# Kernel optimization log

Hardware: AMD Instinct MI355X
Metric: run time of the kernel (lower is better)

## Reference

```python
import jax, jax.numpy as jnp
import numpy as np

N_QUBITS = 8
N_CYCLES = 4
N_GATES = 10
MEAS_QUBITS = (3, 7)
BATCH = 16384


def _apply_ry_batched(state, angles, w):
    # angles: [B] per-example RY angle on wire w. state: [B,2,...,2]
    half = angles * 0.5
    c = jnp.cos(half).astype(jnp.complex64)
    s = jnp.sin(half).astype(jnp.complex64)
    U = jnp.stack([jnp.stack([c, -s], -1), jnp.stack([s, c], -1)], -2)  # [B,2,2]
    st = jnp.moveaxis(state, w + 1, -1)
    st = jnp.einsum('bij,b...j->b...i', U, st)
    return jnp.moveaxis(st, -1, w + 1)


def _apply_cnot(state, c, t):
    st = jnp.moveaxis(state, (c + 1, t + 1), (-2, -1))
    st = jnp.concatenate([st[..., 0:1, :], st[..., 1:2, ::-1]], axis=-2)
    return jnp.moveaxis(st, (-2, -1), (c + 1, t + 1))


def _apply_crx(state, theta, c, t):
    # CRX: RX(theta) on target when control=1 (torchquantum convention)
    half = theta * 0.5
    co = jnp.cos(half).astype(jnp.complex64)
    si = (-1j * jnp.sin(half)).astype(jnp.complex64)
    st = jnp.moveaxis(state, (c + 1, t + 1), (-2, -1))
    s1 = st[..., 1, :]
    s1 = jnp.stack([co * s1[..., 0] + si * s1[..., 1],
                    si * s1[..., 0] + co * s1[..., 1]], -1)
    st = jnp.concatenate([st[..., 0:1, :], s1[..., None, :]], axis=-2)
    return jnp.moveaxis(st, (-2, -1), (c + 1, t + 1))


def _expval_z(probs, w):
    axes = tuple(a for a in range(1, N_QUBITS + 1) if a != w + 1)
    m = jnp.sum(probs, axis=axes)  # [B,2]
    return m[:, 0] - m[:, 1]


def _forward(x, crx_theta, w1, b1, w2, b2):
    B = x.shape[0]
    state = jnp.zeros((B, 2 ** N_QUBITS), jnp.complex64).at[:, 0].set(1.0)
    state = state.reshape((B,) + (2,) * N_QUBITS)
    # encoding ansatz: per cycle, RY(x[:,cyc,q]) on each qubit + CNOT ring
    for cyc in range(N_CYCLES):
        for q in range(N_QUBITS):
            state = _apply_ry_batched(state, x[:, cyc, q], q)
        for q in range(N_QUBITS):
            state = _apply_cnot(state, q, (q + 1) % N_QUBITS)
    # trainable CRX layer
    for i in range(N_GATES):
        state = _apply_crx(state, crx_theta[i], i % N_QUBITS, (i + 1) % N_QUBITS)
    probs = jnp.abs(state) ** 2  # real, [B,2,...,2]
    feats = jnp.stack([_expval_z(probs, q) for q in MEAS_QUBITS], -1)  # [B,2]
    h = jnp.tanh(feats @ w1.T + b1)
    return jax.nn.sigmoid(h @ w2.T + b2)  # [B,1]


def setup_inputs() -> dict:
    key = jax.random.key(0)
    ks = jax.random.split(key, 6)
    x = jax.random.normal(ks[0], (BATCH, N_CYCLES, N_QUBITS), jnp.float32)
    crx_theta = jax.random.normal(ks[1], (N_GATES,), jnp.float32) * 0.1
    w1 = jax.random.normal(ks[2], (10, 2), jnp.float32) * (1.0 / np.sqrt(2.0))
    b1 = jnp.zeros((10,), jnp.float32)
    w2 = jax.random.normal(ks[3], (1, 10), jnp.float32) * (1.0 / np.sqrt(10.0))
    b2 = jnp.zeros((1,), jnp.float32)
    return {"x": x, "crx_theta": crx_theta, "w1": w1, "b1": b1, "w2": w2, "b2": b2}


def reference(x, crx_theta, w1, b1, w2, b2):
    return _forward(x, crx_theta, w1, b1, w2, b2)
```

## Files before the change

kernel.cpp:

```cpp
#include <hip/hip_runtime.h>
#include <math.h>


typedef float f2 __attribute__((ext_vector_type(2)));

#define RLF(v, i) __int_as_float(__builtin_amdgcn_readlane(__float_as_int(v), (i)))
#define BPF(a, v) __int_as_float(__builtin_amdgcn_ds_bpermute((a), __float_as_int(v)))
#define DPPF(v, ctrl) __uint_as_float((unsigned)__builtin_amdgcn_update_dpp( \
    0, (int)__float_as_uint(v), (ctrl), 0xf, 0xf, true))

__device__ __forceinline__ f2 mk2(float a, float b) { f2 r; r.x = a; r.y = b; return r; }

#define PX1S(v)  DPPF((v), 0xB1)
#define PX2S(v)  DPPF((v), 0x4E)
#define PX4S(v)  DPPF(DPPF((v), 0x141), 0x1B)
#define PX8S(v)  DPPF((v), 0x128)

#define PX1(v)  mk2(PX1S((v).x), PX1S((v).y))
#define PX2(v)  mk2(PX2S((v).x), PX2S((v).y))
#define PX4(v)  mk2(PX4S((v).x), PX4S((v).y))
#define PX8(v)  mk2(PX8S((v).x), PX8S((v).y))
#define PX16(v) mk2(BPF(a16, (v).x), BPF(a16, (v).y))
#define PX32(v) mk2(BPF(a32, (v).x), BPF(a32, (v).y))
#define FMA2(a, b, c) __builtin_elementwise_fma((a), (b), (c))

__global__ __launch_bounds__(256, 8) void vqcnn_wave(
    const float* __restrict__ x,
    const float* __restrict__ crx_theta,
    const float* __restrict__ w1,
    const float* __restrict__ b1,
    const float* __restrict__ w2,
    const float* __restrict__ b2,
    float* __restrict__ out)
{
    const int lane = threadIdx.x & 63;
    const int bA   = blockIdx.x * 8 + (threadIdx.x >> 6) * 2;
    const int bB   = bA + 1;

    float cvA, svA, cvB, svB;
    {
        float angA = 0.0f, angB = 0.0f;
        if (lane < 32) {
            angA = x[bA * 32 + lane];
            angB = x[bB * 32 + lane];
        } else if (lane < 42) {
            angA = angB = crx_theta[lane - 32];
        }
        __sincosf(0.5f * angA, &svA, &cvA);
        __sincosf(0.5f * angB, &svB, &cvB);
    }

    const int a16 = (lane ^ 16) << 2;
    const int a32 = (lane ^ 32) << 2;
    const int g4  = (lane ^ (lane >> 1)) << 2;
    const int g4b = g4 ^ (48 << 2);
    const bool l0 = (lane & 1) != 0;

#define RL2C(i) mk2(RLF(cvA, (i)), RLF(cvB, (i)))
#define RL2S(i) mk2(RLF(svA, (i)), RLF(svB, (i)))

    f2 vv0, vv1, vv2, vv3;
    {
#define SEL0(bit, i) ((lane & (bit)) ? RL2S(i) : RL2C(i))
        f2 L = SEL0(32, 0) * SEL0(16, 1);
        L = L * SEL0(8, 2);
        L = L * SEL0(4, 3);
        L = L * SEL0(2, 4);
        L = L * SEL0(1, 5);
        const f2 c6 = RL2C(6), s6 = RL2S(6);
        const f2 c7 = RL2C(7), s7 = RL2S(7);
        const f2 Lc6 = L * c6, Ls6 = L * s6;
        vv0 = Lc6 * c7; vv1 = Lc6 * s7; vv2 = Ls6 * c7; vv3 = Ls6 * s7;
    }

#define RING() {                                                             \
    const f2 t0a = PXG(vv0), t0b = PXG(vv2);                                 \
    const f2 t1a = PXGB(vv1), t1b = PXGB(vv3);                               \
    const f2 t2a = PXG(vv3), t2b = PXG(vv1);                                 \
    const f2 t3a = PXGB(vv2), t3b = PXGB(vv0);                               \
    vv0 = l0 ? t0b : t0a;  vv1 = l0 ? t1b : t1a;                             \
    vv2 = l0 ? t2b : t2a;  vv3 = l0 ? t3b : t3a; }
#define PXG(v)  mk2(BPF(g4,  (v).x), BPF(g4,  (v).y))
#define PXGB(v) mk2(BPF(g4b, (v).x), BPF(g4b, (v).y))
    RING()

#define RY_G(ia, mask, PART) {                                               \
    const f2 c = RL2C(ia), s = RL2S(ia);                                     \
    const f2 ss = (lane & (mask)) ? s : -s;                                  \
    const f2 p0 = PART(vv0), p1 = PART(vv1);                                 \
    const f2 p2 = PART(vv2), p3 = PART(vv3);                                 \
    vv0 = FMA2(ss, p0, c * vv0); vv1 = FMA2(ss, p1, c * vv1);                \
    vv2 = FMA2(ss, p2, c * vv2); vv3 = FMA2(ss, p3, c * vv3); }

#define RY_SLOT1(ia) {                                                       \
    const f2 c = RL2C(ia), s = RL2S(ia);                                     \
    const f2 n0 = c*vv0 - s*vv2, n2 = FMA2(s, vv0, c*vv2);                   \
    const f2 n1 = c*vv1 - s*vv3, n3 = FMA2(s, vv1, c*vv3);                   \
    vv0 = n0; vv1 = n1; vv2 = n2; vv3 = n3; }

#define RY_SLOT0(ia) {                                                       \
    const f2 c = RL2C(ia), s = RL2S(ia);                                     \
    const f2 n0 = c*vv0 - s*vv1, n1 = FMA2(s, vv0, c*vv1);                   \
    const f2 n2 = c*vv2 - s*vv3, n3 = FMA2(s, vv2, c*vv3);                   \
    vv0 = n0; vv1 = n1; vv2 = n2; vv3 = n3; }

    #pragma unroll
    for (int cyc = 1; cyc < 4; ++cyc) {
        const int base = cyc * 8;
        RY_G(base + 0, 32, PX32)
        RY_G(base + 1, 16, PX16)
        RY_G(base + 2,  8, PX8)
        RY_G(base + 3,  4, PX4)
        RY_G(base + 4,  2, PX2)
        RY_G(base + 5,  1, PX1)
        RY_SLOT1(base + 6)
        RY_SLOT0(base + 7)
        RING()
    }

    f2 rr0 = vv0, rr1 = vv1, rr2 = vv2, rr3 = vv3;
    f2 ii0 = {0.f, 0.f}, ii1 = {0.f, 0.f}, ii2 = {0.f, 0.f}, ii3 = {0.f, 0.f};

#define CRX_G(gi, cmask, PART) {                                             \
    const f2 c = RL2C(32 + (gi)), s = RL2S(32 + (gi));                       \
    const bool ct = (lane & (cmask)) != 0;                                   \
    f2 pr, pi, nr, ni;                                                       \
    pr = PART(rr0); pi = PART(ii0);                                          \
    nr = FMA2(s, pi, c*rr0); ni = c*ii0 - s*pr;                              \
    rr0 = ct?nr:rr0; ii0 = ct?ni:ii0;                                        \
    pr = PART(rr1); pi = PART(ii1);                                          \
    nr = FMA2(s, pi, c*rr1); ni = c*ii1 - s*pr;                              \
    rr1 = ct?nr:rr1; ii1 = ct?ni:ii1;                                        \
    pr = PART(rr2); pi = PART(ii2);                                          \
    nr = FMA2(s, pi, c*rr2); ni = c*ii2 - s*pr;                              \
    rr2 = ct?nr:rr2; ii2 = ct?ni:ii2;                                        \
    pr = PART(rr3); pi = PART(ii3);                                          \
    nr = FMA2(s, pi, c*rr3); ni = c*ii3 - s*pr;                              \
    rr3 = ct?nr:rr3; ii3 = ct?ni:ii3; }

    CRX_G(0, 32, PX16)
    CRX_G(1, 16, PX8)
    CRX_G(2,  8, PX4)
    CRX_G(3,  4, PX2)
    CRX_G(4,  2, PX1)
    {
        const f2 c = RL2C(37), s = RL2S(37);
        const f2 nr0 = FMA2(s, ii2, c*rr0), ni0 = c*ii0 - s*rr2;
        const f2 nr2 = FMA2(s, ii0, c*rr2), ni2 = c*ii2 - s*rr0;
        const f2 nr1 = FMA2(s, ii3, c*rr1), ni1 = c*ii1 - s*rr3;
        const f2 nr3 = FMA2(s, ii1, c*rr3), ni3 = c*ii3 - s*rr1;
        rr0 = l0?nr0:rr0; ii0 = l0?ni0:ii0; rr1 = l0?nr1:rr1; ii1 = l0?ni1:ii1;
        rr2 = l0?nr2:rr2; ii2 = l0?ni2:ii2; rr3 = l0?nr3:rr3; ii3 = l0?ni3:ii3;
    }
    {
        const f2 c = RL2C(38), s = RL2S(38);
        const f2 nr2 = FMA2(s, ii3, c*rr2), ni2 = c*ii2 - s*rr3;
        const f2 nr3 = FMA2(s, ii2, c*rr3), ni3 = c*ii3 - s*rr2;
        rr2 = nr2; ii2 = ni2; rr3 = nr3; ii3 = ni3;
    }
    {
        const f2 c = RL2C(39), s = RL2S(39);
        const f2 pr1 = PX32(rr1), pi1 = PX32(ii1);
        const f2 pr3 = PX32(rr3), pi3 = PX32(ii3);
        const f2 nr1 = FMA2(s, pi1, c*rr1), ni1 = c*ii1 - s*pr1;
        const f2 nr3 = FMA2(s, pi3, c*rr3), ni3 = c*ii3 - s*pr3;
        rr1 = nr1; ii1 = ni1; rr3 = nr3; ii3 = ni3;
    }
    CRX_G(8, 32, PX16)
    CRX_G(9, 16, PX8)

    const f2 p0 = FMA2(rr0, rr0, ii0*ii0), p1 = FMA2(rr1, rr1, ii1*ii1);
    const f2 p2 = FMA2(rr2, rr2, ii2*ii2), p3 = FMA2(rr3, rr3, ii3*ii3);
    const f2 sum = (p0 + p1) + (p2 + p3);
    f2 vq7 = (p0 + p2) - (p1 + p3);
    f2 vq3 = (lane & 4) ? -sum : sum;
    vq3 = vq3 + PX1(vq3);   vq7 = vq7 + PX1(vq7);
    vq3 = vq3 + PX2(vq3);   vq7 = vq7 + PX2(vq7);
    vq3 = vq3 + PX4(vq3);   vq7 = vq7 + PX4(vq7);
    vq3 = vq3 + PX8(vq3);   vq7 = vq7 + PX8(vq7);
    vq3 = vq3 + PX16(vq3);  vq7 = vq7 + PX16(vq7);
    vq3 = vq3 + PX32(vq3);  vq7 = vq7 + PX32(vq7);

    float wa = 0.f, wb = 0.f, bb = 0.f, wc = 0.f;
    if (lane < 10) {
        wa = w1[2 * lane];
        wb = w1[2 * lane + 1];
        bb = b1[lane];
        wc = w2[lane];
    }
    const f2 z = FMA2(mk2(wa, wa), vq3, FMA2(mk2(wb, wb), vq7, mk2(bb, bb)));
    const f2 e = mk2(__expf(2.0f * z.x), __expf(2.0f * z.y));
    const f2 h = mk2(1.0f - 2.0f * __builtin_amdgcn_rcpf(e.x + 1.0f),
                     1.0f - 2.0f * __builtin_amdgcn_rcpf(e.y + 1.0f));
    f2 acc = mk2(wc, wc) * h;
    acc = acc + PX1(acc);
    acc = acc + PX2(acc);
    acc = acc + PX4(acc);
    acc = acc + PX8(acc);
    if (lane == 0) {
        const float bias = b2[0];
        out[bA] = __builtin_amdgcn_rcpf(1.0f + __expf(-(acc.x + bias)));
        out[bB] = __builtin_amdgcn_rcpf(1.0f + __expf(-(acc.y + bias)));
    }
}

extern "C" void kernel_launch(void* const* d_in, const int* in_sizes, int n_in,
                              void* d_out, int out_size, void* d_ws, size_t ws_size,
                              hipStream_t stream) {
    const float* x         = (const float*)d_in[0];
    const float* crx_theta = (const float*)d_in[1];
    const float* w1        = (const float*)d_in[2];
    const float* b1        = (const float*)d_in[3];
    const float* w2        = (const float*)d_in[4];
    const float* b2        = (const float*)d_in[5];
    float* out = (float*)d_out;

    const int B = in_sizes[0] / 32;
    vqcnn_wave<<<B / 8, 256, 0, stream>>>(x, crx_theta, w1, b1, w2, b2, out);
}
```

Before: 81.48 us.

## Process four batch examples per wavefront and cut ring permute selects

Each wavefront now simulates four examples instead of two, held as two interleaved f2 state sets. This doubles independent instruction streams for latency hiding and halves the grid size. The CNOT ring now selects sources by lane-parity before the bpermute, so each ring step issues half as many bpermutes. The cost is higher register pressure (launch bounds drop to 4 waves/EU) and fewer total wavefronts to fill the GPU.

```diff
diff --git a/kernel.cpp b/kernel.cpp
--- a/kernel.cpp
+++ b/kernel.cpp
@@ -24,7 +24,7 @@
 #define PX32(v) mk2(BPF(a32, (v).x), BPF(a32, (v).y))
 #define FMA2(a, b, c) __builtin_elementwise_fma((a), (b), (c))
 
-__global__ __launch_bounds__(256, 8) void vqcnn_wave(
+__global__ __launch_bounds__(256, 4) void vqcnn_wave(
     const float* __restrict__ x,
     const float* __restrict__ crx_theta,
     const float* __restrict__ w1,
@@ -34,152 +34,210 @@
     float* __restrict__ out)
 {
     const int lane = threadIdx.x & 63;
-    const int bA   = blockIdx.x * 8 + (threadIdx.x >> 6) * 2;
-    const int bB   = bA + 1;
-
-    float cvA, svA, cvB, svB;
-    {
-        float angA = 0.0f, angB = 0.0f;
+    const int bA   = blockIdx.x * 16 + (threadIdx.x >> 6) * 4;
+
+    float cvA, svA, cvB, svB, cvC, svC, cvD, svD;
+    {
+        float aA = 0.f, aB = 0.f, aC = 0.f, aD = 0.f;
         if (lane < 32) {
-            angA = x[bA * 32 + lane];
-            angB = x[bB * 32 + lane];
+            aA = x[(bA + 0) * 32 + lane];
+            aB = x[(bA + 1) * 32 + lane];
+            aC = x[(bA + 2) * 32 + lane];
+            aD = x[(bA + 3) * 32 + lane];
         } else if (lane < 42) {
-            angA = angB = crx_theta[lane - 32];
+            aA = aB = aC = aD = crx_theta[lane - 32];
         }
-        __sincosf(0.5f * angA, &svA, &cvA);
-        __sincosf(0.5f * angB, &svB, &cvB);
+        __sincosf(0.5f * aA, &svA, &cvA);
+        __sincosf(0.5f * aB, &svB, &cvB);
+        __sincosf(0.5f * aC, &svC, &cvC);
+        __sincosf(0.5f * aD, &svD, &cvD);
     }
 
     const int a16 = (lane ^ 16) << 2;
     const int a32 = (lane ^ 32) << 2;
     const int g4  = (lane ^ (lane >> 1)) << 2;
     const int g4b = g4 ^ (48 << 2);
-    const bool l0 = (lane & 1) != 0;
-
-#define RL2C(i) mk2(RLF(cvA, (i)), RLF(cvB, (i)))
-#define RL2S(i) mk2(RLF(svA, (i)), RLF(svB, (i)))
-
-    f2 vv0, vv1, vv2, vv3;
-    {
-#define SEL0(bit, i) ((lane & (bit)) ? RL2S(i) : RL2C(i))
-        f2 L = SEL0(32, 0) * SEL0(16, 1);
-        L = L * SEL0(8, 2);
-        L = L * SEL0(4, 3);
-        L = L * SEL0(2, 4);
-        L = L * SEL0(1, 5);
-        const f2 c6 = RL2C(6), s6 = RL2S(6);
-        const f2 c7 = RL2C(7), s7 = RL2S(7);
-        const f2 Lc6 = L * c6, Ls6 = L * s6;
-        vv0 = Lc6 * c7; vv1 = Lc6 * s7; vv2 = Ls6 * c7; vv3 = Ls6 * s7;
-    }
-
-#define RING() {                                                             \
-    const f2 t0a = PXG(vv0), t0b = PXG(vv2);                                 \
-    const f2 t1a = PXGB(vv1), t1b = PXGB(vv3);                               \
-    const f2 t2a = PXG(vv3), t2b = PXG(vv1);                                 \
-    const f2 t3a = PXGB(vv2), t3b = PXGB(vv0);                               \
-    vv0 = l0 ? t0b : t0a;  vv1 = l0 ? t1b : t1a;                             \
-    vv2 = l0 ? t2b : t2a;  vv3 = l0 ? t3b : t3a; }
-#define PXG(v)  mk2(BPF(g4,  (v).x), BPF(g4,  (v).y))
-#define PXGB(v) mk2(BPF(g4b, (v).x), BPF(g4b, (v).y))
-    RING()
-
-#define RY_G(ia, mask, PART) {                                               \
-    const f2 c = RL2C(ia), s = RL2S(ia);                                     \
-    const f2 ss = (lane & (mask)) ? s : -s;                                  \
-    const f2 p0 = PART(vv0), p1 = PART(vv1);                                 \
-    const f2 p2 = PART(vv2), p3 = PART(vv3);                                 \
-    vv0 = FMA2(ss, p0, c * vv0); vv1 = FMA2(ss, p1, c * vv1);                \
-    vv2 = FMA2(ss, p2, c * vv2); vv3 = FMA2(ss, p3, c * vv3); }
-
-#define RY_SLOT1(ia) {                                                       \
-    const f2 c = RL2C(ia), s = RL2S(ia);                                     \
-    const f2 n0 = c*vv0 - s*vv2, n2 = FMA2(s, vv0, c*vv2);                   \
-    const f2 n1 = c*vv1 - s*vv3, n3 = FMA2(s, vv1, c*vv3);                   \
-    vv0 = n0; vv1 = n1; vv2 = n2; vv3 = n3; }
-
-#define RY_SLOT0(ia) {                                                       \
-    const f2 c = RL2C(ia), s = RL2S(ia);                                     \
-    const f2 n0 = c*vv0 - s*vv1, n1 = FMA2(s, vv0, c*vv1);                   \
-    const f2 n2 = c*vv2 - s*vv3, n3 = FMA2(s, vv2, c*vv3);                   \
-    vv0 = n0; vv1 = n1; vv2 = n2; vv3 = n3; }
+    const bool psel = (__builtin_popcount(lane) & 1) != 0;
+
+#define RLCu(i) mk2(RLF(cvA, (i)), RLF(cvB, (i)))
+#define RLSu(i) mk2(RLF(svA, (i)), RLF(svB, (i)))
+#define RLCw(i) mk2(RLF(cvC, (i)), RLF(cvD, (i)))
+#define RLSw(i) mk2(RLF(svC, (i)), RLF(svD, (i)))
+
+    f2 vv0u, vv1u, vv2u, vv3u, vv0w, vv1w, vv2w, vv3w;
+    {
+#define SELu(bit, i) ((lane & (bit)) ? RLSu(i) : RLCu(i))
+#define SELw(bit, i) ((lane & (bit)) ? RLSw(i) : RLCw(i))
+        f2 Lu = SELu(32, 0) * SELu(16, 1);
+        f2 Lw = SELw(32, 0) * SELw(16, 1);
+        Lu = Lu * SELu(8, 2);   Lw = Lw * SELw(8, 2);
+        Lu = Lu * SELu(4, 3);   Lw = Lw * SELw(4, 3);
+        Lu = Lu * SELu(2, 4);   Lw = Lw * SELw(2, 4);
+        Lu = Lu * SELu(1, 5);   Lw = Lw * SELw(1, 5);
+        const f2 c6u = RLCu(6), s6u = RLSu(6), c7u = RLCu(7), s7u = RLSu(7);
+        const f2 c6w = RLCw(6), s6w = RLSw(6), c7w = RLCw(7), s7w = RLSw(7);
+        const f2 Lcu = Lu * c6u, Lsu = Lu * s6u;
+        const f2 Lcw = Lw * c6w, Lsw = Lw * s6w;
+        vv0u = Lcu * c7u; vv1u = Lcu * s7u; vv2u = Lsu * c7u; vv3u = Lsu * s7u;
+        vv0w = Lcw * c7w; vv1w = Lcw * s7w; vv2w = Lsw * c7w; vv3w = Lsw * s7w;
+    }
+
+#define RING2() {                                                            \
+    const f2 z0u = psel ? vv2u : vv0u,  z0w = psel ? vv2w : vv0w;            \
+    const f2 z1u = psel ? vv3u : vv1u,  z1w = psel ? vv3w : vv1w;            \
+    const f2 z2u = psel ? vv1u : vv3u,  z2w = psel ? vv1w : vv3w;            \
+    const f2 z3u = psel ? vv0u : vv2u,  z3w = psel ? vv0w : vv2w;            \
+    vv0u = mk2(BPF(g4,  z0u.x), BPF(g4,  z0u.y));                            \
+    vv0w = mk2(BPF(g4,  z0w.x), BPF(g4,  z0w.y));                            \
+    vv1u = mk2(BPF(g4b, z1u.x), BPF(g4b, z1u.y));                            \
+    vv1w = mk2(BPF(g4b, z1w.x), BPF(g4b, z1w.y));                            \
+    vv2u = mk2(BPF(g4,  z2u.x), BPF(g4,  z2u.y));                            \
+    vv2w = mk2(BPF(g4,  z2w.x), BPF(g4,  z2w.y));                            \
+    vv3u = mk2(BPF(g4b, z3u.x), BPF(g4b, z3u.y));                            \
+    vv3w = mk2(BPF(g4b, z3w.x), BPF(g4b, z3w.y)); }
+    RING2()
+
+#define RY_G2(ia, mask, PART) {                                              \
+    const f2 cu = RLCu(ia), su = RLSu(ia);                                   \
+    const f2 cw = RLCw(ia), sw = RLSw(ia);                                   \
+    const f2 ssu = (lane & (mask)) ? su : -su;                               \
+    const f2 ssw = (lane & (mask)) ? sw : -sw;                               \
+    const f2 p0u = PART(vv0u), p0w = PART(vv0w);                             \
+    const f2 p1u = PART(vv1u), p1w = PART(vv1w);                             \
+    const f2 p2u = PART(vv2u), p2w = PART(vv2w);                             \
+    const f2 p3u = PART(vv3u), p3w = PART(vv3w);                             \
+    vv0u = FMA2(ssu, p0u, cu * vv0u);  vv0w = FMA2(ssw, p0w, cw * vv0w);     \
+    vv1u = FMA2(ssu, p1u, cu * vv1u);  vv1w = FMA2(ssw, p1w, cw * vv1w);     \
+    vv2u = FMA2(ssu, p2u, cu * vv2u);  vv2w = FMA2(ssw, p2w, cw * vv2w);     \
+    vv3u = FMA2(ssu, p3u, cu * vv3u);  vv3w = FMA2(ssw, p3w, cw * vv3w); }
+
+#define RY_SLOT1_2(ia) {                                                     \
+    const f2 cu = RLCu(ia), su = RLSu(ia);                                   \
+    const f2 cw = RLCw(ia), sw = RLSw(ia);                                   \
+    const f2 n0u = cu*vv0u - su*vv2u, n2u = FMA2(su, vv0u, cu*vv2u);         \
+    const f2 n0w = cw*vv0w - sw*vv2w, n2w = FMA2(sw, vv0w, cw*vv2w);         \
+    const f2 n1u = cu*vv1u - su*vv3u, n3u = FMA2(su, vv1u, cu*vv3u);         \
+    const f2 n1w = cw*vv1w - sw*vv3w, n3w = FMA2(sw, vv1w, cw*vv3w);         \
+    vv0u = n0u; vv1u = n1u; vv2u = n2u; vv3u = n3u;                          \
+    vv0w = n0w; vv1w = n1w; vv2w = n2w; vv3w = n3w; }
+
+#define RY_SLOT0_2(ia) {                                                     \
+    const f2 cu = RLCu(ia), su = RLSu(ia);                                   \
+    const f2 cw = RLCw(ia), sw = RLSw(ia);                                   \
+    const f2 n0u = cu*vv0u - su*vv1u, n1u = FMA2(su, vv0u, cu*vv1u);         \
+    const f2 n0w = cw*vv0w - sw*vv1w, n1w = FMA2(sw, vv0w, cw*vv1w);         \
+    const f2 n2u = cu*vv2u - su*vv3u, n3u = FMA2(su, vv2u, cu*vv3u);         \
+    const f2 n2w = cw*vv2w - sw*vv3w, n3w = FMA2(sw, vv2w, cw*vv3w);         \
+    vv0u = n0u; vv1u = n1u; vv2u = n2u; vv3u = n3u;                          \
+    vv0w = n0w; vv1w = n1w; vv2w = n2w; vv3w = n3w; }
 
     #pragma unroll
     for (int cyc = 1; cyc < 4; ++cyc) {
         const int base = cyc * 8;
-        RY_G(base + 0, 32, PX32)
-        RY_G(base + 1, 16, PX16)
-        RY_G(base + 2,  8, PX8)
-        RY_G(base + 3,  4, PX4)
-        RY_G(base + 4,  2, PX2)
-        RY_G(base + 5,  1, PX1)
-        RY_SLOT1(base + 6)
-        RY_SLOT0(base + 7)
-        RING()
-    }
-
-    f2 rr0 = vv0, rr1 = vv1, rr2 = vv2, rr3 = vv3;
-    f2 ii0 = {0.f, 0.f}, ii1 = {0.f, 0.f}, ii2 = {0.f, 0.f}, ii3 = {0.f, 0.f};
-
-#define CRX_G(gi, cmask, PART) {                                             \
-    const f2 c = RL2C(32 + (gi)), s = RL2S(32 + (gi));                       \
+        RY_G2(base + 0, 32, PX32)
+        RY_G2(base + 1, 16, PX16)
+        RY_G2(base + 2,  8, PX8)
+        RY_G2(base + 3,  4, PX4)
+        RY_G2(base + 4,  2, PX2)
+        RY_G2(base + 5,  1, PX1)
+        RY_SLOT1_2(base + 6)
+        RY_SLOT0_2(base + 7)
+        RING2()
+    }
+
+    f2 rr0u = vv0u, rr1u = vv1u, rr2u = vv2u, rr3u = vv3u;
+    f2 rr0w = vv0w, rr1w = vv1w, rr2w = vv2w, rr3w = vv3w;
+    f2 ii0u = {0,0}, ii1u = {0,0}, ii2u = {0,0}, ii3u = {0,0};
+    f2 ii0w = {0,0}, ii1w = {0,0}, ii2w = {0,0}, ii3w = {0,0};
+
+#define CRX_PAIR(cS, sS, ct, rr, ii, PART, S)                                \
+    { const f2 pr = PART(rr##S); const f2 pi = PART(ii##S);                  \
+      const f2 nr = FMA2(sS, pi, cS*rr##S);                                  \
+      const f2 ni = cS*ii##S - sS*pr;                                        \
+      rr##S = ct ? nr : rr##S; ii##S = ct ? ni : ii##S; }
+
+#define CRX_G2(gi, cmask, PART) {                                            \
+    const f2 cu = RLCu(32 + (gi)), su = RLSu(32 + (gi));                     \
+    const f2 cw = RLCw(32 + (gi)), sw = RLSw(32 + (gi));                     \
     const bool ct = (lane & (cmask)) != 0;                                   \
-    f2 pr, pi, nr, ni;                                                       \
-    pr = PART(rr0); pi = PART(ii0);                                          \
-    nr = FMA2(s, pi, c*rr0); ni = c*ii0 - s*pr;                              \
-    rr0 = ct?nr:rr0; ii0 = ct?ni:ii0;                                        \
-    pr = PART(rr1); pi = PART(ii1);                                          \
-    nr = FMA2(s, pi, c*rr1); ni = c*ii1 - s*pr;                              \
-    rr1 = ct?nr:rr1; ii1 = ct?ni:ii1;                                        \
-    pr = PART(rr2); pi = PART(ii2);                                          \
-    nr = FMA2(s, pi, c*rr2); ni = c*ii2 - s*pr;                              \
-    rr2 = ct?nr:rr2; ii2 = ct?ni:ii2;                                        \
-    pr = PART(rr3); pi = PART(ii3);                                          \
-    nr = FMA2(s, pi, c*rr3); ni = c*ii3 - s*pr;                              \
-    rr3 = ct?nr:rr3; ii3 = ct?ni:ii3; }
-
-    CRX_G(0, 32, PX16)
-    CRX_G(1, 16, PX8)
-    CRX_G(2,  8, PX4)
-    CRX_G(3,  4, PX2)
-    CRX_G(4,  2, PX1)
-    {
-        const f2 c = RL2C(37), s = RL2S(37);
-        const f2 nr0 = FMA2(s, ii2, c*rr0), ni0 = c*ii0 - s*rr2;
-        const f2 nr2 = FMA2(s, ii0, c*rr2), ni2 = c*ii2 - s*rr0;
-        const f2 nr1 = FMA2(s, ii3, c*rr1), ni1 = c*ii1 - s*rr3;
-        const f2 nr3 = FMA2(s, ii1, c*rr3), ni3 = c*ii3 - s*rr1;
-        rr0 = l0?nr0:rr0; ii0 = l0?ni0:ii0; rr1 = l0?nr1:rr1; ii1 = l0?ni1:ii1;
-        rr2 = l0?nr2:rr2; ii2 = l0?ni2:ii2; rr3 = l0?nr3:rr3; ii3 = l0?ni3:ii3;
-    }
-    {
-        const f2 c = RL2C(38), s = RL2S(38);
-        const f2 nr2 = FMA2(s, ii3, c*rr2), ni2 = c*ii2 - s*rr3;
-        const f2 nr3 = FMA2(s, ii2, c*rr3), ni3 = c*ii3 - s*rr2;
-        rr2 = nr2; ii2 = ni2; rr3 = nr3; ii3 = ni3;
-    }
-    {
-        const f2 c = RL2C(39), s = RL2S(39);
-        const f2 pr1 = PX32(rr1), pi1 = PX32(ii1);
-        const f2 pr3 = PX32(rr3), pi3 = PX32(ii3);
-        const f2 nr1 = FMA2(s, pi1, c*rr1), ni1 = c*ii1 - s*pr1;
-        const f2 nr3 = FMA2(s, pi3, c*rr3), ni3 = c*ii3 - s*pr3;
-        rr1 = nr1; ii1 = ni1; rr3 = nr3; ii3 = ni3;
-    }
-    CRX_G(8, 32, PX16)
-    CRX_G(9, 16, PX8)
-
-    const f2 p0 = FMA2(rr0, rr0, ii0*ii0), p1 = FMA2(rr1, rr1, ii1*ii1);
-    const f2 p2 = FMA2(rr2, rr2, ii2*ii2), p3 = FMA2(rr3, rr3, ii3*ii3);
-    const f2 sum = (p0 + p1) + (p2 + p3);
-    f2 vq7 = (p0 + p2) - (p1 + p3);
-    f2 vq3 = (lane & 4) ? -sum : sum;
-    vq3 = vq3 + PX1(vq3);   vq7 = vq7 + PX1(vq7);
-    vq3 = vq3 + PX2(vq3);   vq7 = vq7 + PX2(vq7);
-    vq3 = vq3 + PX4(vq3);   vq7 = vq7 + PX4(vq7);
-    vq3 = vq3 + PX8(vq3);   vq7 = vq7 + PX8(vq7);
-    vq3 = vq3 + PX16(vq3);  vq7 = vq7 + PX16(vq7);
-    vq3 = vq3 + PX32(vq3);  vq7 = vq7 + PX32(vq7);
+    CRX_PAIR(cu, su, ct, rr0, ii0, PART, u)                                  \
+    CRX_PAIR(cw, sw, ct, rr0, ii0, PART, w)                                  \
+    CRX_PAIR(cu, su, ct, rr1, ii1, PART, u)                                  \
+    CRX_PAIR(cw, sw, ct, rr1, ii1, PART, w)                                  \
+    CRX_PAIR(cu, su, ct, rr2, ii2, PART, u)                                  \
+    CRX_PAIR(cw, sw, ct, rr2, ii2, PART, w)                                  \
+    CRX_PAIR(cu, su, ct, rr3, ii3, PART, u)                                  \
+    CRX_PAIR(cw, sw, ct, rr3, ii3, PART, w) }
+
+    CRX_G2(0, 32, PX16)
+    CRX_G2(1, 16, PX8)
+    CRX_G2(2,  8, PX4)
+    CRX_G2(3,  4, PX2)
+    CRX_G2(4,  2, PX1)
+    {
+        const bool l0 = (lane & 1) != 0;
+        const f2 cu = RLCu(37), su = RLSu(37);
+        const f2 cw = RLCw(37), sw = RLSw(37);
+        const f2 nr0u = FMA2(su, ii2u, cu*rr0u), ni0u = cu*ii0u - su*rr2u;
+        const f2 nr0w = FMA2(sw, ii2w, cw*rr0w), ni0w = cw*ii0w - sw*rr2w;
+        const f2 nr2u = FMA2(su, ii0u, cu*rr2u), ni2u = cu*ii2u - su*rr0u;
+        const f2 nr2w = FMA2(sw, ii0w, cw*rr2w), ni2w = cw*ii2w - sw*rr0w;
+        const f2 nr1u = FMA2(su, ii3u, cu*rr1u), ni1u = cu*ii1u - su*rr3u;
+        const f2 nr1w = FMA2(sw, ii3w, cw*rr1w), ni1w = cw*ii1w - sw*rr3w;
+        const f2 nr3u = FMA2(su, ii1u, cu*rr3u), ni3u = cu*ii3u - su*rr1u;
+        const f2 nr3w = FMA2(sw, ii1w, cw*rr3w), ni3w = cw*ii3w - sw*rr1w;
+        rr0u = l0?nr0u:rr0u; ii0u = l0?ni0u:ii0u; rr0w = l0?nr0w:rr0w; ii0w = l0?ni0w:ii0w;
+        rr1u = l0?nr1u:rr1u; ii1u = l0?ni1u:ii1u; rr1w = l0?nr1w:rr1w; ii1w = l0?ni1w:ii1w;
+        rr2u = l0?nr2u:rr2u; ii2u = l0?ni2u:ii2u; rr2w = l0?nr2w:rr2w; ii2w = l0?ni2w:ii2w;
+        rr3u = l0?nr3u:rr3u; ii3u = l0?ni3u:ii3u; rr3w = l0?nr3w:rr3w; ii3w = l0?ni3w:ii3w;
+    }
+    {
+        const f2 cu = RLCu(38), su = RLSu(38);
+        const f2 cw = RLCw(38), sw = RLSw(38);
+        const f2 nr2u = FMA2(su, ii3u, cu*rr2u), ni2u = cu*ii2u - su*rr3u;
+        const f2 nr2w = FMA2(sw, ii3w, cw*rr2w), ni2w = cw*ii2w - sw*rr3w;
+        const f2 nr3u = FMA2(su, ii2u, cu*rr3u), ni3u = cu*ii3u - su*rr2u;
+        const f2 nr3w = FMA2(sw, ii2w, cw*rr3w), ni3w = cw*ii3w - sw*rr2w;
+        rr2u = nr2u; ii2u = ni2u; rr3u = nr3u; ii3u = ni3u;
+        rr2w = nr2w; ii2w = ni2w; rr3w = nr3w; ii3w = ni3w;
+    }
+    {
+        const f2 cu = RLCu(39), su = RLSu(39);
+        const f2 cw = RLCw(39), sw = RLSw(39);
+        const f2 pr1u = PX32(rr1u), pi1u = PX32(ii1u);
+        const f2 pr1w = PX32(rr1w), pi1w = PX32(ii1w);
+        const f2 pr3u = PX32(rr3u), pi3u = PX32(ii3u);
+        const f2 pr3w = PX32(rr3w), pi3w = PX32(ii3w);
+        rr1u = FMA2(su, pi1u, cu*rr1u); ii1u = cu*ii1u - su*pr1u;
+        rr1w = FMA2(sw, pi1w, cw*rr1w); ii1w = cw*ii1w - sw*pr1w;
+        rr3u = FMA2(su, pi3u, cu*rr3u); ii3u = cu*ii3u - su*pr3u;
+        rr3w = FMA2(sw, pi3w, cw*rr3w); ii3w = cw*ii3w - sw*pr3w;
+    }
+    CRX_G2(8, 32, PX16)
+    CRX_G2(9, 16, PX8)
+
+    const f2 p0u = FMA2(rr0u, rr0u, ii0u*ii0u), p1u = FMA2(rr1u, rr1u, ii1u*ii1u);
+    const f2 p2u = FMA2(rr2u, rr2u, ii2u*ii2u), p3u = FMA2(rr3u, rr3u, ii3u*ii3u);
+    const f2 p0w = FMA2(rr0w, rr0w, ii0w*ii0w), p1w = FMA2(rr1w, rr1w, ii1w*ii1w);
+    const f2 p2w = FMA2(rr2w, rr2w, ii2w*ii2w), p3w = FMA2(rr3w, rr3w, ii3w*ii3w);
+    const f2 sumu = (p0u + p1u) + (p2u + p3u);
+    const f2 sumw = (p0w + p1w) + (p2w + p3w);
+    f2 vq7u = (p0u + p2u) - (p1u + p3u);
+    f2 vq7w = (p0w + p2w) - (p1w + p3w);
+    f2 vq3u = (lane & 4) ? -sumu : sumu;
+    f2 vq3w = (lane & 4) ? -sumw : sumw;
+    vq3u = vq3u + PX1(vq3u);   vq7u = vq7u + PX1(vq7u);
+    vq3w = vq3w + PX1(vq3w);   vq7w = vq7w + PX1(vq7w);
+    vq3u = vq3u + PX2(vq3u);   vq7u = vq7u + PX2(vq7u);
+    vq3w = vq3w + PX2(vq3w);   vq7w = vq7w + PX2(vq7w);
+    vq3u = vq3u + PX4(vq3u);   vq7u = vq7u + PX4(vq7u);
+    vq3w = vq3w + PX4(vq3w);   vq7w = vq7w + PX4(vq7w);
+    vq3u = vq3u + PX8(vq3u);   vq7u = vq7u + PX8(vq7u);
+    vq3w = vq3w + PX8(vq3w);   vq7w = vq7w + PX8(vq7w);
+    vq3u = vq3u + PX16(vq3u);  vq7u = vq7u + PX16(vq7u);
+    vq3w = vq3w + PX16(vq3w);  vq7w = vq7w + PX16(vq7w);
+    vq3u = vq3u + PX32(vq3u);  vq7u = vq7u + PX32(vq7u);
+    vq3w = vq3w + PX32(vq3w);  vq7w = vq7w + PX32(vq7w);
 
     float wa = 0.f, wb = 0.f, bb = 0.f, wc = 0.f;
     if (lane < 10) {
@@ -188,19 +246,27 @@
         bb = b1[lane];
         wc = w2[lane];
     }
-    const f2 z = FMA2(mk2(wa, wa), vq3, FMA2(mk2(wb, wb), vq7, mk2(bb, bb)));
-    const f2 e = mk2(__expf(2.0f * z.x), __expf(2.0f * z.y));
-    const f2 h = mk2(1.0f - 2.0f * __builtin_amdgcn_rcpf(e.x + 1.0f),
-                     1.0f - 2.0f * __builtin_amdgcn_rcpf(e.y + 1.0f));
-    f2 acc = mk2(wc, wc) * h;
-    acc = acc + PX1(acc);
-    acc = acc + PX2(acc);
-    acc = acc + PX4(acc);
-    acc = acc + PX8(acc);
+    const f2 wa2 = mk2(wa, wa), wb2 = mk2(wb, wb), bb2 = mk2(bb, bb);
+    const f2 zu = FMA2(wa2, vq3u, FMA2(wb2, vq7u, bb2));
+    const f2 zw = FMA2(wa2, vq3w, FMA2(wb2, vq7w, bb2));
+    const f2 eu = mk2(__expf(2.0f * zu.x), __expf(2.0f * zu.y));
+    const f2 ew = mk2(__expf(2.0f * zw.x), __expf(2.0f * zw.y));
+    const f2 hu = mk2(1.0f - 2.0f * __builtin_amdgcn_rcpf(eu.x + 1.0f),
+                      1.0f - 2.0f * __builtin_amdgcn_rcpf(eu.y + 1.0f));
+    const f2 hw = mk2(1.0f - 2.0f * __builtin_amdgcn_rcpf(ew.x + 1.0f),
+                      1.0f - 2.0f * __builtin_amdgcn_rcpf(ew.y + 1.0f));
+    f2 au = mk2(wc, wc) * hu;
+    f2 aw = mk2(wc, wc) * hw;
+    au = au + PX1(au);  aw = aw + PX1(aw);
+    au = au + PX2(au);  aw = aw + PX2(aw);
+    au = au + PX4(au);  aw = aw + PX4(aw);
+    au = au + PX8(au);  aw = aw + PX8(aw);
     if (lane == 0) {
         const float bias = b2[0];
-        out[bA] = __builtin_amdgcn_rcpf(1.0f + __expf(-(acc.x + bias)));
-        out[bB] = __builtin_amdgcn_rcpf(1.0f + __expf(-(acc.y + bias)));
+        out[bA + 0] = __builtin_amdgcn_rcpf(1.0f + __expf(-(au.x + bias)));
+        out[bA + 1] = __builtin_amdgcn_rcpf(1.0f + __expf(-(au.y + bias)));
+        out[bA + 2] = __builtin_amdgcn_rcpf(1.0f + __expf(-(aw.x + bias)));
+        out[bA + 3] = __builtin_amdgcn_rcpf(1.0f + __expf(-(aw.y + bias)));
     }
 }
 
@@ -216,5 +282,5 @@
     float* out = (float*)d_out;
 
     const int B = in_sizes[0] / 32;
-    vqcnn_wave<<<B / 8, 256, 0, stream>>>(x, crx_theta, w1, b1, w2, b2, out);
+    vqcnn_wave<<<B / 16, 256, 0, stream>>>(x, crx_theta, w1, b1, w2, b2, out);
 }
```

Measured after the change: 82.50 us. Within noise of the previous version (+1.2%).
